# Performance work log

Hardware: AMD Instinct MI355X
Metric: run time of the kernel (lower is better)

Reference implementation:

```python
import jax, jax.numpy as jnp
import numpy as np
from jax import lax

B, D, H, STEPS = 16384, 256, 256, 25


def setup_inputs() -> dict:
    key = jax.random.key(0)
    k1, k2, k3, k4 = jax.random.split(key, 4)
    s1 = 1.0 / np.sqrt(D)
    s2 = 1.0 / np.sqrt(H)
    return {
        "z0": jax.random.normal(k1, (B, D), dtype=jnp.float32),
        "t_range": jnp.linspace(0.0, 1.0, STEPS, dtype=jnp.float32),
        "W1": jax.random.normal(k2, (D, H), dtype=jnp.float32) * s1,
        "b1": jnp.zeros((H,), dtype=jnp.float32),
        "wt": jax.random.normal(k3, (H,), dtype=jnp.float32) * 0.1,
        "W2": jax.random.normal(k4, (H, D), dtype=jnp.float32) * s2,
        "b2": jnp.zeros((D,), dtype=jnp.float32),
    }


def reference(z0, t_range, W1, b1, wt, W2, b2):
    # Euler solver: zt <- zt + dt * f(zt, t) for every t in t_range
    # (matches euler_solver: note it steps at ALL 25 grid points, incl. t_end)
    dt = t_range[1] - t_range[0]

    def dynamics(z, t):
        h = jnp.tanh(z @ W1 + b1 + t * wt)  # [B, H]
        return h @ W2 + b2                   # [B, D]

    def step(z, t):
        return z + dt * dynamics(z, t), None

    zT, _ = lax.scan(step, z0, t_range)
    return zT
```

## Files before the change

### kernel.cpp

```cpp
#include <hip/hip_runtime.h>

typedef short bf16x8 __attribute__((ext_vector_type(8)));
typedef float f32x4  __attribute__((ext_vector_type(4)));

#define NSTEP 25
#define SROW  264
#define LDSB  (32 * SROW)

__device__ __forceinline__ unsigned short f2bf(float x) {
    union { float f; unsigned int u; } v; v.f = x;
    unsigned int r = v.u + 0x7FFFu + ((v.u >> 16) & 1u);
    return (unsigned short)(r >> 16);
}

#if __has_builtin(__builtin_amdgcn_cvt_pk_bf16_f32)
typedef __bf16 bfv2 __attribute__((ext_vector_type(2)));
__device__ __forceinline__ unsigned int pk2bf(float a, float b) {
    union { bfv2 v; unsigned int u; } c;
    c.v = __builtin_amdgcn_cvt_pk_bf16_f32(a, b);
    return c.u;
}
#else
__device__ __forceinline__ unsigned int pk2bf(float a, float b) {
    return (unsigned int)f2bf(a) | ((unsigned int)f2bf(b) << 16);
}
#endif

#if __has_builtin(__builtin_amdgcn_exp2f)
#define EXP2F __builtin_amdgcn_exp2f
#else
#define EXP2F exp2f
#endif

#define C2LOG2E 2.8853900817779268f

__device__ __forceinline__ float tanh_pre(float y, float btc) {
    float e = EXP2F(fmaf(y, C2LOG2E, btc));
    return 1.0f - 2.0f * __builtin_amdgcn_rcpf(e + 1.0f);
}

__global__ void prep_all(const float* __restrict__ W1,
                         const float* __restrict__ W2,
                         const float* __restrict__ b2,
                         const float* __restrict__ t_range,
                         unsigned short* __restrict__ Wr,
                         unsigned short* __restrict__ W21r,
                         float* __restrict__ c1)
{
    __shared__ float row[256];
    int b = blockIdx.x;
    if (b < 257) {
        int i = b, j = threadIdx.x;
        row[j] = (i < 256) ? W2[i * 256 + j] : b2[j];
        __syncthreads();
        float a0 = 0.f, a1 = 0.f, a2 = 0.f, a3 = 0.f;
#pragma unroll
        for (int d = 0; d < 256; d += 16) {
            float w[16];
#pragma unroll
            for (int u = 0; u < 16; ++u) w[u] = W1[(d + u) * 256 + j];
#pragma unroll
            for (int u = 0; u < 16; u += 4) {
                a0 = fmaf(row[d + u + 0], w[u + 0], a0);
                a1 = fmaf(row[d + u + 1], w[u + 1], a1);
                a2 = fmaf(row[d + u + 2], w[u + 2], a2);
                a3 = fmaf(row[d + u + 3], w[u + 3], a3);
            }
        }
        float acc = (a0 + a1) + (a2 + a3);
        if (i < 256) {
            float dt = t_range[1] - t_range[0];
            int p  = (i & ~31) | ((i & 15) << 1) | ((i >> 4) & 1);
            int kc = p >> 5, q = (p >> 3) & 3, jj = p & 7;
            W21r[kc * 8192 + j * 32 + q * 8 + jj] = f2bf(dt * acc);
        } else {
            c1[j] = acc;
        }
    } else {
        int bb = b - 257;
        const float* src = (bb < 256) ? W1 : W2;
        unsigned short* dst = Wr + ((bb < 256) ? 0 : 65536);
        int k = bb & 255;
        int n = threadIdx.x;
        int p  = (k & ~31) | ((k & 15) << 1) | ((k >> 4) & 1);
        int kc = p >> 5, q = (p >> 3) & 3, jj = p & 7;
        dst[kc * 8192 + n * 32 + q * 8 + jj] = f2bf(src[k * 256 + n]);
    }
}

__global__ __launch_bounds__(512, 4) void ode_main(
    const float* __restrict__ z0,
    const float* __restrict__ t_range,
    const float* __restrict__ b1,
    const float* __restrict__ wt,
    const float* __restrict__ b2,
    const unsigned short* __restrict__ W1r,
    const unsigned short* __restrict__ W2r,
    const unsigned short* __restrict__ W21r,
    const float* __restrict__ c1,
    float* __restrict__ out)
{
    __shared__ __align__(16) unsigned short As[2 * LDSB];

    const int tid  = threadIdx.x;
    const int wave = tid >> 6;
    const int lane = tid & 63;
    const int q    = lane >> 4;
    const int l15  = lane & 15;
    const int row0 = blockIdx.x * 32;
    const int n0   = wave * 32;

    const float dt = t_range[1] - t_range[0];

    float btc[2], dbtc[2];
#pragma unroll
    for (int tt = 0; tt < 2; ++tt) {
        int n = n0 + tt * 16 + l15;
        btc[tt]  = b1[n] * C2LOG2E;
        dbtc[tt] = dt * (wt[n] + c1[n]) * C2LOG2E;
    }

#pragma unroll
    for (int band = 0; band < 2; ++band)
#pragma unroll
        for (int r = 0; r < 4; ++r) {
            int m = band * 16 + q * 4 + r;
            const float* zr = &z0[(row0 + m) * 256 + n0];
            *(unsigned int*)&As[m * SROW + n0 + l15 * 2] =
                pk2bf(zr[l15], zr[16 + l15]);
        }
    __syncthreads();

    f32x4 y[2][2];
#pragma unroll
    for (int band = 0; band < 2; ++band)
#pragma unroll
        for (int tt = 0; tt < 2; ++tt) y[band][tt] = f32x4{0.f, 0.f, 0.f, 0.f};
#pragma unroll
    for (int kc = 0; kc < 8; ++kc) {
        bf16x8 a[2];
#pragma unroll
        for (int band = 0; band < 2; ++band)
            a[band] = *(const bf16x8*)&As[(band * 16 + l15) * SROW + kc * 32 + q * 8];
#pragma unroll
        for (int tt = 0; tt < 2; ++tt) {
            bf16x8 bb = *(const bf16x8*)&W1r[kc * 8192 + (n0 + tt * 16 + l15) * 32 + q * 8];
#pragma unroll
            for (int band = 0; band < 2; ++band)
                y[band][tt] = __builtin_amdgcn_mfma_f32_16x16x32_bf16(
                    a[band], bb, y[band][tt], 0, 0, 0);
        }
    }

    bf16x8 w21f[8][2];
#pragma unroll
    for (int kc = 0; kc < 8; ++kc)
#pragma unroll
        for (int tt = 0; tt < 2; ++tt)
            w21f[kc][tt] = *(const bf16x8*)&W21r[kc * 8192 + (n0 + tt * 16 + l15) * 32 + q * 8];

    f32x4 S[2][2];
#pragma unroll
    for (int band = 0; band < 2; ++band)
#pragma unroll
        for (int tt = 0; tt < 2; ++tt) S[band][tt] = f32x4{0.f, 0.f, 0.f, 0.f};

    for (int s = 0; s < NSTEP - 1; ++s) {
        const int buf = ((s + 1) & 1) * LDSB;
#pragma unroll
        for (int band = 0; band < 2; ++band)
#pragma unroll
            for (int r = 0; r < 4; ++r) {
                int m = band * 16 + q * 4 + r;
                float h0 = tanh_pre(y[band][0][r], btc[0]);
                float h1 = tanh_pre(y[band][1][r], btc[1]);
                S[band][0][r] += h0; S[band][1][r] += h1;
                *(unsigned int*)&As[buf + m * SROW + n0 + l15 * 2] = pk2bf(h0, h1);
            }
        __syncthreads();

#pragma unroll
        for (int kc = 0; kc < 8; ++kc) {
            bf16x8 a[2];
#pragma unroll
            for (int band = 0; band < 2; ++band)
                a[band] = *(const bf16x8*)&As[buf + (band * 16 + l15) * SROW + kc * 32 + q * 8];
#pragma unroll
            for (int band = 0; band < 2; ++band)
#pragma unroll
                for (int tt = 0; tt < 2; ++tt)
                    y[band][tt] = __builtin_amdgcn_mfma_f32_16x16x32_bf16(
                        a[band], w21f[kc][tt], y[band][tt], 0, 0, 0);
        }

#pragma unroll
        for (int tt = 0; tt < 2; ++tt) btc[tt] += dbtc[tt];
    }

#pragma unroll
    for (int band = 0; band < 2; ++band)
#pragma unroll
        for (int r = 0; r < 4; ++r)
#pragma unroll
            for (int tt = 0; tt < 2; ++tt)
                S[band][tt][r] += tanh_pre(y[band][tt][r], btc[tt]);

    {
        const int buf = LDSB;
#pragma unroll
        for (int band = 0; band < 2; ++band)
#pragma unroll
            for (int r = 0; r < 4; ++r) {
                int m = band * 16 + q * 4 + r;
                *(unsigned int*)&As[buf + m * SROW + n0 + l15 * 2] =
                    pk2bf(S[band][0][r], S[band][1][r]);
            }
        __syncthreads();

        f32x4 acc[2][2];
#pragma unroll
        for (int band = 0; band < 2; ++band)
#pragma unroll
            for (int tt = 0; tt < 2; ++tt) acc[band][tt] = f32x4{0.f, 0.f, 0.f, 0.f};
#pragma unroll
        for (int kc = 0; kc < 8; ++kc) {
            bf16x8 a[2];
#pragma unroll
            for (int band = 0; band < 2; ++band)
                a[band] = *(const bf16x8*)&As[buf + (band * 16 + l15) * SROW + kc * 32 + q * 8];
#pragma unroll
            for (int tt = 0; tt < 2; ++tt) {
                bf16x8 bb = *(const bf16x8*)&W2r[kc * 8192 + (n0 + tt * 16 + l15) * 32 + q * 8];
#pragma unroll
                for (int band = 0; band < 2; ++band)
                    acc[band][tt] = __builtin_amdgcn_mfma_f32_16x16x32_bf16(
                        a[band], bb, acc[band][tt], 0, 0, 0);
            }
        }

        const float cb2 = (float)NSTEP * dt;
#pragma unroll
        for (int band = 0; band < 2; ++band)
#pragma unroll
            for (int tt = 0; tt < 2; ++tt) {
                float b2v = b2[n0 + tt * 16 + l15];
#pragma unroll
                for (int r = 0; r < 4; ++r) {
                    int idx = (row0 + band * 16 + q * 4 + r) * 256 + n0 + tt * 16 + l15;
                    out[idx] = z0[idx] + dt * acc[band][tt][r] + cb2 * b2v;
                }
            }
    }
}

extern "C" void kernel_launch(void* const* d_in, const int* in_sizes, int n_in,
                              void* d_out, int out_size, void* d_ws, size_t ws_size,
                              hipStream_t stream) {
    const float* z0      = (const float*)d_in[0];
    const float* t_range = (const float*)d_in[1];
    const float* W1      = (const float*)d_in[2];
    const float* b1      = (const float*)d_in[3];
    const float* wt      = (const float*)d_in[4];
    const float* W2      = (const float*)d_in[5];
    const float* b2      = (const float*)d_in[6];

    unsigned short* Wr = (unsigned short*)d_ws;
    unsigned short* W1r  = Wr;
    unsigned short* W2r  = Wr + 65536;
    unsigned short* W21r = Wr + 131072;
    float*          c1   = (float*)(Wr + 196608);

    prep_all<<<769, 256, 0, stream>>>(W1, W2, b2, t_range, Wr, W21r, c1);
    ode_main<<<512, 512, 0, stream>>>(z0, t_range, b1, wt, b2,
                                      W1r, W2r, W21r, c1, (float*)d_out);
}
```

Before: 145.9 us.

## Unroll step loop by two, raise MFMA priority, stagger block start

```diff
diff --git a/kernel.cpp b/kernel.cpp
--- a/kernel.cpp
+++ b/kernel.cpp
@@ -88,6 +88,37 @@
     }
 }
 
+#define STEP_BODY(BUF)                                                          \
+  {                                                                             \
+    const int buf = (BUF);                                                      \
+    _Pragma("unroll")                                                           \
+    for (int band = 0; band < 2; ++band)                                        \
+      _Pragma("unroll")                                                         \
+      for (int r = 0; r < 4; ++r) {                                             \
+        int m = band * 16 + q * 4 + r;                                          \
+        float h0 = tanh_pre(y[band][0][r], btc[0]);                             \
+        float h1 = tanh_pre(y[band][1][r], btc[1]);                             \
+        S[band][0][r] += h0; S[band][1][r] += h1;                               \
+        *(unsigned int*)&As[buf + m * SROW + n0 + l15 * 2] = pk2bf(h0, h1);     \
+      }                                                                         \
+    btc[0] += dbtc[0]; btc[1] += dbtc[1];                                       \
+    __syncthreads();                                                            \
+    __builtin_amdgcn_s_setprio(1);                                              \
+    _Pragma("unroll")                                                           \
+    for (int kc = 0; kc < 8; ++kc) {                                            \
+      bf16x8 a0 = *(const bf16x8*)&As[buf + l15 * SROW + kc * 32 + q * 8];      \
+      bf16x8 a1 = *(const bf16x8*)&As[buf + (16 + l15) * SROW + kc * 32 + q * 8];\
+      _Pragma("unroll")                                                         \
+      for (int tt = 0; tt < 2; ++tt) {                                          \
+        y[0][tt] = __builtin_amdgcn_mfma_f32_16x16x32_bf16(a0, w21f[kc][tt],    \
+                                                           y[0][tt], 0, 0, 0); \
+        y[1][tt] = __builtin_amdgcn_mfma_f32_16x16x32_bf16(a1, w21f[kc][tt],    \
+                                                           y[1][tt], 0, 0, 0); \
+      }                                                                         \
+    }                                                                           \
+    __builtin_amdgcn_s_setprio(0);                                              \
+  }
+
 __global__ __launch_bounds__(512, 4) void ode_main(
     const float* __restrict__ z0,
     const float* __restrict__ t_range,
@@ -165,36 +196,12 @@
 #pragma unroll
         for (int tt = 0; tt < 2; ++tt) S[band][tt] = f32x4{0.f, 0.f, 0.f, 0.f};
 
-    for (int s = 0; s < NSTEP - 1; ++s) {
-        const int buf = ((s + 1) & 1) * LDSB;
-#pragma unroll
-        for (int band = 0; band < 2; ++band)
-#pragma unroll
-            for (int r = 0; r < 4; ++r) {
-                int m = band * 16 + q * 4 + r;
-                float h0 = tanh_pre(y[band][0][r], btc[0]);
-                float h1 = tanh_pre(y[band][1][r], btc[1]);
-                S[band][0][r] += h0; S[band][1][r] += h1;
-                *(unsigned int*)&As[buf + m * SROW + n0 + l15 * 2] = pk2bf(h0, h1);
-            }
-        __syncthreads();
-
-#pragma unroll
-        for (int kc = 0; kc < 8; ++kc) {
-            bf16x8 a[2];
-#pragma unroll
-            for (int band = 0; band < 2; ++band)
-                a[band] = *(const bf16x8*)&As[buf + (band * 16 + l15) * SROW + kc * 32 + q * 8];
-#pragma unroll
-            for (int band = 0; band < 2; ++band)
-#pragma unroll
-                for (int tt = 0; tt < 2; ++tt)
-                    y[band][tt] = __builtin_amdgcn_mfma_f32_16x16x32_bf16(
-                        a[band], w21f[kc][tt], y[band][tt], 0, 0, 0);
-        }
-
-#pragma unroll
-        for (int tt = 0; tt < 2; ++tt) btc[tt] += dbtc[tt];
+    if ((blockIdx.x >> 8) & 1) __builtin_amdgcn_s_sleep(22);
+
+#pragma unroll 1
+    for (int it = 0; it < (NSTEP - 1) / 2; ++it) {
+        STEP_BODY(LDSB)
+        STEP_BODY(0)
     }
 
 #pragma unroll
```

After: 152.2 us. 1.04x slower.

## Software-pipeline tanh of one row band with MFMAs of the other band

Applied to the files above, without the earlier changes.

```diff
diff --git a/kernel.cpp b/kernel.cpp
--- a/kernel.cpp
+++ b/kernel.cpp
@@ -88,6 +88,26 @@
     }
 }
 
+#define REGION(MB, TB, RBUF, SBUF, BTC)                                         \
+  {                                                                             \
+    _Pragma("unroll")                                                           \
+    for (int kc = 0; kc < 8; ++kc) {                                            \
+      bf16x8 a = *(const bf16x8*)&As[(RBUF) + ((MB)*16 + l15) * SROW + kc * 32 + q * 8]; \
+      y[MB][0] = __builtin_amdgcn_mfma_f32_16x16x32_bf16(a, w21f[kc][0], y[MB][0], 0, 0, 0); \
+      y[MB][1] = __builtin_amdgcn_mfma_f32_16x16x32_bf16(a, w21f[kc][1], y[MB][1], 0, 0, 0); \
+      if (kc & 1) {                                                             \
+        int r = kc >> 1;                                                        \
+        int m = (TB)*16 + q * 4 + r;                                            \
+        float h0 = tanh_pre(y[TB][0][r], BTC[0]);                               \
+        float h1 = tanh_pre(y[TB][1][r], BTC[1]);                               \
+        S[TB][0][r] += h0; S[TB][1][r] += h1;                                   \
+        *(unsigned int*)&As[(SBUF) + m * SROW + n0 + l15 * 2] = pk2bf(h0, h1);  \
+      }                                                                         \
+    }                                                                           \
+    BTC[0] += dbtc[0]; BTC[1] += dbtc[1];                                       \
+    __syncthreads();                                                            \
+  }
+
 __global__ __launch_bounds__(512, 4) void ode_main(
     const float* __restrict__ z0,
     const float* __restrict__ t_range,
@@ -103,20 +123,20 @@
     __shared__ __align__(16) unsigned short As[2 * LDSB];
 
     const int tid  = threadIdx.x;
-    const int wave = tid >> 6;
     const int lane = tid & 63;
     const int q    = lane >> 4;
     const int l15  = lane & 15;
     const int row0 = blockIdx.x * 32;
-    const int n0   = wave * 32;
+    const int n0   = (tid >> 6) * 32;
 
     const float dt = t_range[1] - t_range[0];
 
-    float btc[2], dbtc[2];
+    float btc0[2], btc1[2], dbtc[2];
 #pragma unroll
     for (int tt = 0; tt < 2; ++tt) {
         int n = n0 + tt * 16 + l15;
-        btc[tt]  = b1[n] * C2LOG2E;
+        btc0[tt] = b1[n] * C2LOG2E;
+        btc1[tt] = btc0[tt];
         dbtc[tt] = dt * (wt[n] + c1[n]) * C2LOG2E;
     }
 
@@ -151,6 +171,7 @@
                     a[band], bb, y[band][tt], 0, 0, 0);
         }
     }
+    __syncthreads();
 
     bf16x8 w21f[8][2];
 #pragma unroll
@@ -165,48 +186,33 @@
 #pragma unroll
         for (int tt = 0; tt < 2; ++tt) S[band][tt] = f32x4{0.f, 0.f, 0.f, 0.f};
 
+#pragma unroll
+    for (int r = 0; r < 4; ++r) {
+        int m = q * 4 + r;
+        float h0 = tanh_pre(y[0][0][r], btc0[0]);
+        float h1 = tanh_pre(y[0][1][r], btc0[1]);
+        S[0][0][r] += h0; S[0][1][r] += h1;
+        *(unsigned int*)&As[m * SROW + n0 + l15 * 2] = pk2bf(h0, h1);
+    }
+    btc0[0] += dbtc[0]; btc0[1] += dbtc[1];
+    __syncthreads();
+
+#pragma unroll 1
     for (int s = 0; s < NSTEP - 1; ++s) {
-        const int buf = ((s + 1) & 1) * LDSB;
-#pragma unroll
-        for (int band = 0; band < 2; ++band)
-#pragma unroll
-            for (int r = 0; r < 4; ++r) {
-                int m = band * 16 + q * 4 + r;
-                float h0 = tanh_pre(y[band][0][r], btc[0]);
-                float h1 = tanh_pre(y[band][1][r], btc[1]);
-                S[band][0][r] += h0; S[band][1][r] += h1;
-                *(unsigned int*)&As[buf + m * SROW + n0 + l15 * 2] = pk2bf(h0, h1);
-            }
-        __syncthreads();
-
-#pragma unroll
-        for (int kc = 0; kc < 8; ++kc) {
-            bf16x8 a[2];
-#pragma unroll
-            for (int band = 0; band < 2; ++band)
-                a[band] = *(const bf16x8*)&As[buf + (band * 16 + l15) * SROW + kc * 32 + q * 8];
-#pragma unroll
-            for (int band = 0; band < 2; ++band)
-#pragma unroll
-                for (int tt = 0; tt < 2; ++tt)
-                    y[band][tt] = __builtin_amdgcn_mfma_f32_16x16x32_bf16(
-                        a[band], w21f[kc][tt], y[band][tt], 0, 0, 0);
-        }
-
-#pragma unroll
-        for (int tt = 0; tt < 2; ++tt) btc[tt] += dbtc[tt];
-    }
-
-#pragma unroll
-    for (int band = 0; band < 2; ++band)
-#pragma unroll
-        for (int r = 0; r < 4; ++r)
-#pragma unroll
-            for (int tt = 0; tt < 2; ++tt)
-                S[band][tt][r] += tanh_pre(y[band][tt][r], btc[tt]);
+        const int bs = (s & 1) * LDSB;
+        const int bn = ((s + 1) & 1) * LDSB;
+        REGION(0, 1, bs, bs, btc1)
+        REGION(1, 0, bs, bn, btc0)
+    }
+
+#pragma unroll
+    for (int r = 0; r < 4; ++r)
+#pragma unroll
+        for (int tt = 0; tt < 2; ++tt)
+            S[1][tt][r] += tanh_pre(y[1][tt][r], btc1[tt]);
 
     {
-        const int buf = LDSB;
+        const int buf = 0;
 #pragma unroll
         for (int band = 0; band < 2; ++band)
 #pragma unroll
```

Result: slower. 148.9 us (+2.0%).

## Repartition ODE kernel to 16-row blocks with 16 waves each owning 16 columns

Applied to the files above, without the earlier changes.

```diff
diff --git a/kernel.cpp b/kernel.cpp
--- a/kernel.cpp
+++ b/kernel.cpp
@@ -5,7 +5,7 @@
 
 #define NSTEP 25
 #define SROW  264
-#define LDSB  (32 * SROW)
+#define LDSB  (16 * SROW)
 
 __device__ __forceinline__ unsigned short f2bf(float x) {
     union { float f; unsigned int u; } v; v.f = x;
@@ -15,15 +15,13 @@
 
 #if __has_builtin(__builtin_amdgcn_cvt_pk_bf16_f32)
 typedef __bf16 bfv2 __attribute__((ext_vector_type(2)));
-__device__ __forceinline__ unsigned int pk2bf(float a, float b) {
+__device__ __forceinline__ unsigned short f2bf1(float a) {
     union { bfv2 v; unsigned int u; } c;
-    c.v = __builtin_amdgcn_cvt_pk_bf16_f32(a, b);
-    return c.u;
+    c.v = __builtin_amdgcn_cvt_pk_bf16_f32(a, a);
+    return (unsigned short)c.u;
 }
 #else
-__device__ __forceinline__ unsigned int pk2bf(float a, float b) {
-    return (unsigned int)f2bf(a) | ((unsigned int)f2bf(b) << 16);
-}
+__device__ __forceinline__ unsigned short f2bf1(float a) { return f2bf(a); }
 #endif
 
 #if __has_builtin(__builtin_amdgcn_exp2f)
@@ -88,7 +86,7 @@
     }
 }
 
-__global__ __launch_bounds__(512, 4) void ode_main(
+__global__ __launch_bounds__(1024, 8) void ode_main(
     const float* __restrict__ z0,
     const float* __restrict__ t_range,
     const float* __restrict__ b1,
@@ -107,149 +105,83 @@
     const int lane = tid & 63;
     const int q    = lane >> 4;
     const int l15  = lane & 15;
-    const int row0 = blockIdx.x * 32;
-    const int n0   = wave * 32;
+    const int row0 = blockIdx.x * 16;
+    const int n0   = wave * 16;
+    const int g    = wave >> 1, half = wave & 1;
+
+    unsigned short* const       hw = &As[(q * 4) * SROW + g * 32 + 2 * l15 + half];
+    const unsigned short* const ar = &As[l15 * SROW + q * 8];
 
     const float dt = t_range[1] - t_range[0];
 
-    float btc[2], dbtc[2];
-#pragma unroll
-    for (int tt = 0; tt < 2; ++tt) {
-        int n = n0 + tt * 16 + l15;
-        btc[tt]  = b1[n] * C2LOG2E;
-        dbtc[tt] = dt * (wt[n] + c1[n]) * C2LOG2E;
-    }
-
-#pragma unroll
-    for (int band = 0; band < 2; ++band)
-#pragma unroll
-        for (int r = 0; r < 4; ++r) {
-            int m = band * 16 + q * 4 + r;
-            const float* zr = &z0[(row0 + m) * 256 + n0];
-            *(unsigned int*)&As[m * SROW + n0 + l15 * 2] =
-                pk2bf(zr[l15], zr[16 + l15]);
-        }
+    const int n = n0 + l15;
+    float btc  = b1[n] * C2LOG2E;
+    float dbtc = dt * (wt[n] + c1[n]) * C2LOG2E;
+
+#pragma unroll
+    for (int r = 0; r < 4; ++r)
+        hw[r * SROW] = f2bf1(z0[(row0 + q * 4 + r) * 256 + n]);
     __syncthreads();
 
-    f32x4 y[2][2];
-#pragma unroll
-    for (int band = 0; band < 2; ++band)
-#pragma unroll
-        for (int tt = 0; tt < 2; ++tt) y[band][tt] = f32x4{0.f, 0.f, 0.f, 0.f};
+    f32x4 y = f32x4{0.f, 0.f, 0.f, 0.f};
 #pragma unroll
     for (int kc = 0; kc < 8; ++kc) {
-        bf16x8 a[2];
-#pragma unroll
-        for (int band = 0; band < 2; ++band)
-            a[band] = *(const bf16x8*)&As[(band * 16 + l15) * SROW + kc * 32 + q * 8];
-#pragma unroll
-        for (int tt = 0; tt < 2; ++tt) {
-            bf16x8 bb = *(const bf16x8*)&W1r[kc * 8192 + (n0 + tt * 16 + l15) * 32 + q * 8];
-#pragma unroll
-            for (int band = 0; band < 2; ++band)
-                y[band][tt] = __builtin_amdgcn_mfma_f32_16x16x32_bf16(
-                    a[band], bb, y[band][tt], 0, 0, 0);
-        }
-    }
-
-    bf16x8 w21f[8][2];
+        bf16x8 a  = *(const bf16x8*)&ar[kc * 32];
+        bf16x8 bb = *(const bf16x8*)&W1r[kc * 8192 + n * 32 + q * 8];
+        y = __builtin_amdgcn_mfma_f32_16x16x32_bf16(a, bb, y, 0, 0, 0);
+    }
+
+    bf16x8 w21f[8];
 #pragma unroll
     for (int kc = 0; kc < 8; ++kc)
-#pragma unroll
-        for (int tt = 0; tt < 2; ++tt)
-            w21f[kc][tt] = *(const bf16x8*)&W21r[kc * 8192 + (n0 + tt * 16 + l15) * 32 + q * 8];
-
-    f32x4 S[2][2];
-#pragma unroll
-    for (int band = 0; band < 2; ++band)
-#pragma unroll
-        for (int tt = 0; tt < 2; ++tt) S[band][tt] = f32x4{0.f, 0.f, 0.f, 0.f};
+        w21f[kc] = *(const bf16x8*)&W21r[kc * 8192 + n * 32 + q * 8];
+
+    f32x4 S = f32x4{0.f, 0.f, 0.f, 0.f};
 
     for (int s = 0; s < NSTEP - 1; ++s) {
         const int buf = ((s + 1) & 1) * LDSB;
 #pragma unroll
-        for (int band = 0; band < 2; ++band)
-#pragma unroll
-            for (int r = 0; r < 4; ++r) {
-                int m = band * 16 + q * 4 + r;
-                float h0 = tanh_pre(y[band][0][r], btc[0]);
-                float h1 = tanh_pre(y[band][1][r], btc[1]);
-                S[band][0][r] += h0; S[band][1][r] += h1;
-                *(unsigned int*)&As[buf + m * SROW + n0 + l15 * 2] = pk2bf(h0, h1);
-            }
+        for (int r = 0; r < 4; ++r) {
+            float h = tanh_pre(y[r], btc);
+            S[r] += h;
+            hw[buf + r * SROW] = f2bf1(h);
+        }
+        btc += dbtc;
         __syncthreads();
 
 #pragma unroll
         for (int kc = 0; kc < 8; ++kc) {
-            bf16x8 a[2];
-#pragma unroll
-            for (int band = 0; band < 2; ++band)
-                a[band] = *(const bf16x8*)&As[buf + (band * 16 + l15) * SROW + kc * 32 + q * 8];
-#pragma unroll
-            for (int band = 0; band < 2; ++band)
-#pragma unroll
-                for (int tt = 0; tt < 2; ++tt)
-                    y[band][tt] = __builtin_amdgcn_mfma_f32_16x16x32_bf16(
-                        a[band], w21f[kc][tt], y[band][tt], 0, 0, 0);
-        }
-
-#pragma unroll
-        for (int tt = 0; tt < 2; ++tt) btc[tt] += dbtc[tt];
-    }
-
-#pragma unroll
-    for (int band = 0; band < 2; ++band)
-#pragma unroll
-        for (int r = 0; r < 4; ++r)
-#pragma unroll
-            for (int tt = 0; tt < 2; ++tt)
-                S[band][tt][r] += tanh_pre(y[band][tt][r], btc[tt]);
+            bf16x8 a = *(const bf16x8*)&ar[buf + kc * 32];
+            y = __builtin_amdgcn_mfma_f32_16x16x32_bf16(a, w21f[kc], y, 0, 0, 0);
+        }
+    }
+
+#pragma unroll
+    for (int r = 0; r < 4; ++r)
+        S[r] += tanh_pre(y[r], btc);
 
     {
         const int buf = LDSB;
 #pragma unroll
-        for (int band = 0; band < 2; ++band)
-#pragma unroll
-            for (int r = 0; r < 4; ++r) {
-                int m = band * 16 + q * 4 + r;
-                *(unsigned int*)&As[buf + m * SROW + n0 + l15 * 2] =
-                    pk2bf(S[band][0][r], S[band][1][r]);
-            }
+        for (int r = 0; r < 4; ++r)
+            hw[buf + r * SROW] = f2bf1(S[r]);
         __syncthreads();
 
-        f32x4 acc[2][2];
-#pragma unroll
-        for (int band = 0; band < 2; ++band)
-#pragma unroll
-            for (int tt = 0; tt < 2; ++tt) acc[band][tt] = f32x4{0.f, 0.f, 0.f, 0.f};
+        f32x4 acc = f32x4{0.f, 0.f, 0.f, 0.f};
 #pragma unroll
         for (int kc = 0; kc < 8; ++kc) {
-            bf16x8 a[2];
-#pragma unroll
-            for (int band = 0; band < 2; ++band)
-                a[band] = *(const bf16x8*)&As[buf + (band * 16 + l15) * SROW + kc * 32 + q * 8];
-#pragma unroll
-            for (int tt = 0; tt < 2; ++tt) {
-                bf16x8 bb = *(const bf16x8*)&W2r[kc * 8192 + (n0 + tt * 16 + l15) * 32 + q * 8];
-#pragma unroll
-                for (int band = 0; band < 2; ++band)
-                    acc[band][tt] = __builtin_amdgcn_mfma_f32_16x16x32_bf16(
-                        a[band], bb, acc[band][tt], 0, 0, 0);
-            }
+            bf16x8 a  = *(const bf16x8*)&ar[buf + kc * 32];
+            bf16x8 bb = *(const bf16x8*)&W2r[kc * 8192 + n * 32 + q * 8];
+            acc = __builtin_amdgcn_mfma_f32_16x16x32_bf16(a, bb, acc, 0, 0, 0);
         }
 
         const float cb2 = (float)NSTEP * dt;
-#pragma unroll
-        for (int band = 0; band < 2; ++band)
-#pragma unroll
-            for (int tt = 0; tt < 2; ++tt) {
-                float b2v = b2[n0 + tt * 16 + l15];
-#pragma unroll
-                for (int r = 0; r < 4; ++r) {
-                    int idx = (row0 + band * 16 + q * 4 + r) * 256 + n0 + tt * 16 + l15;
-                    out[idx] = z0[idx] + dt * acc[band][tt][r] + cb2 * b2v;
-                }
-            }
+        const float b2v = b2[n];
+#pragma unroll
+        for (int r = 0; r < 4; ++r) {
+            int idx = (row0 + q * 4 + r) * 256 + n;
+            out[idx] = z0[idx] + dt * acc[r] + cb2 * b2v;
+        }
     }
 }
 
@@ -271,6 +203,6 @@
     float*          c1   = (float*)(Wr + 196608);
 
     prep_all<<<769, 256, 0, stream>>>(W1, W2, b2, t_range, Wr, W21r, c1);
-    ode_main<<<512, 512, 0, stream>>>(z0, t_range, b1, wt, b2,
-                                      W1r, W2r, W21r, c1, (float*)d_out);
-}
+    ode_main<<<1024, 1024, 0, stream>>>(z0, t_range, b1, wt, b2,
+                                        W1r, W2r, W21r, c1, (float*)d_out);
+}
```

New measurement: 157.7 us. 1.08x slower.
